# Kernel optimization log

Hardware: AMD Instinct MI355X
Metric: run time of the kernel (lower is better)

The kernel has to match this reference:

```python
import jax, jax.numpy as jnp
import numpy as np

MESH_SIZE = 0.01
TEMP = 0.001
T = 4096
HID = (16, 16, 16)


def _triangle_mesh():
    g = np.arange(-1.0, 1.0 + 1e-9, MESH_SIZE, dtype=np.float32)  # 201 pts
    A, B = np.meshgrid(g, g, indexing='ij')  # alpha rows, beta cols
    mask = A >= B                             # Preisach triangle alpha >= beta
    return A[mask].astype(np.float32), B[mask].astype(np.float32)  # [N], [N]


def _constrain(v, lo, hi):
    return lo + (hi - lo) * jax.nn.sigmoid(v)


def setup_inputs() -> dict:
    key = jax.random.key(0)
    ks = jax.random.split(key, 12)
    alpha_np, beta_np = _triangle_mesh()
    N = alpha_np.shape[0]  # 20301

    def xavier(k, fan_in, fan_out):
        b = np.sqrt(6.0 / (fan_in + fan_out)).astype(np.float32)
        return jax.random.uniform(k, (fan_in, fan_out), jnp.float32, -b, b)

    dims = (2,) + HID + (1,)
    params = {}
    for i in range(4):
        params[f'w{i+1}'] = xavier(ks[i], dims[i], dims[i + 1])
        params[f'b{i+1}'] = jnp.zeros((dims[i + 1],), jnp.float32)

    bound = np.sqrt(6.0 / (1 + N)).astype(np.float32)  # xavier_uniform on (1,N)
    init_state_raw = jax.random.uniform(ks[10], (N,), jnp.float32, -bound, bound)

    return dict(
        x=jax.random.normal(ks[11], (T,), jnp.float32),
        alpha_raw=jnp.asarray(alpha_np),
        beta_raw=jnp.asarray(beta_np),
        init_state_raw=init_state_raw,
        m_scale_raw=jnp.asarray(1.0, jnp.float32),
        m_offset_raw=jnp.asarray(1.0, jnp.float32),
        h_scale_raw=jnp.asarray(1.0, jnp.float32),
        **params,
    )


def _get_states(x, alpha, beta, s0, temp):
    # Soft Preisach relay: switch up where u>alpha, down where u<beta, else hold.
    def step(s, u):
        up = jax.nn.sigmoid((u - alpha) / temp)
        dn = jax.nn.sigmoid((beta - u) / temp)
        s_new = up - dn + (1.0 - up) * (1.0 - dn) * s
        return s_new, s_new
    _, states = jax.lax.scan(step, s0, x)
    return states  # [T, N]


def reference(x, alpha_raw, beta_raw, init_state_raw,
              w1, b1, w2, b2, w3, b3, w4, b4,
              m_scale_raw, m_offset_raw, h_scale_raw):
    alpha = alpha_raw  # ConstrainedParameter with no bounds -> identity
    beta = beta_raw
    s0 = jnp.tanh(init_state_raw)  # BinaryParameter (soft binary)

    states = _get_states(x, alpha, beta, s0, TEMP)  # [T, N]

    mesh = jnp.stack([alpha, beta], axis=1)  # [N, 2]
    h = jax.nn.relu(mesh @ w1 + b1)
    h = jax.nn.relu(h @ w2 + b2)
    h = jax.nn.relu(h @ w3 + b3)
    density = jax.nn.sigmoid(h @ w4 + b4)  # [N, 1]
    density = density.T  # [1, N]

    m = jnp.sum(density * states, axis=-1) / jnp.sum(density, axis=-1)  # [T]

    m_scale = _constrain(m_scale_raw, 0.0, 10.0)
    m_offset = _constrain(m_offset_raw, -10.0, 10.0)
    h_scale = _constrain(h_scale_raw, 0.0, 10.0)

    out = m_scale * m + m_offset + h_scale * x  # [T]
    return out, density, states
```

## Files before the change

### kernel.cpp

```cpp
#include <hip/hip_runtime.h>
#include <math.h>

#define NM 20301
#define TT 4096
#define NC 64
#define CH 64
#define NBLK 80
#define SBLK 20
#define NPROW (SBLK * 4)
#define TPH 16
#define NPH (CH / TPH)
#define LOG2E_K 1442.69504f
#define WNEAR 26.0f

__device__ __forceinline__ void relay_step(float ka, float kb, float ku,
                                           float& aa, float& bb) {
    float z1 = fminf(ka - ku, 63.f);
    float z2 = fminf(ku - kb, 63.f);
    float e1 = __builtin_amdgcn_exp2f(z1);
    float e2 = __builtin_amdgcn_exp2f(z2);
    float p1 = 1.f + e1, p2 = 1.f + e2;
    float r  = __builtin_amdgcn_rcpf(p1 * p2);
    aa = (e2 - e1) * r;
    bb = (e1 * e2) * r;
}

__device__ __forceinline__ float wave_reduce_sum(float w) {
    #pragma unroll
    for (int off = 32; off > 0; off >>= 1)
        w += __shfl_down(w, off, 64);
    return w;
}

__global__ __launch_bounds__(256) void density_kernel(
    const float* __restrict__ alpha, const float* __restrict__ beta,
    const float* __restrict__ w1, const float* __restrict__ b1,
    const float* __restrict__ w2, const float* __restrict__ b2,
    const float* __restrict__ w3, const float* __restrict__ b3,
    const float* __restrict__ w4, const float* __restrict__ b4,
    float* __restrict__ density_out, float* __restrict__ densum_parts,
    float* __restrict__ corr)
{
    int n = blockIdx.x * 256 + threadIdx.x;
    if (n < TT) corr[n] = 0.f;
    bool valid = n < NM;
    int nn = valid ? n : NM - 1;
    float a = alpha[nn], b = beta[nn];

    float h1[16], h2[16], h3[16];
    #pragma unroll
    for (int j = 0; j < 16; j++) {
        float v = fmaf(a, w1[j], fmaf(b, w1[16 + j], b1[j]));
        h1[j] = fmaxf(v, 0.f);
    }
    #pragma unroll
    for (int j = 0; j < 16; j++) {
        float v = b2[j];
        #pragma unroll
        for (int k = 0; k < 16; k++) v = fmaf(h1[k], w2[k * 16 + j], v);
        h2[j] = fmaxf(v, 0.f);
    }
    #pragma unroll
    for (int j = 0; j < 16; j++) {
        float v = b3[j];
        #pragma unroll
        for (int k = 0; k < 16; k++) v = fmaf(h2[k], w3[k * 16 + j], v);
        h3[j] = fmaxf(v, 0.f);
    }
    float v = b4[0];
    #pragma unroll
    for (int k = 0; k < 16; k++) v = fmaf(h3[k], w4[k], v);
    float d = 1.f / (1.f + __expf(-v));

    if (valid) density_out[n] = d;
    float wsum = wave_reduce_sum(valid ? d : 0.f);
    __shared__ float ws_[4];
    if ((threadIdx.x & 63) == 0) ws_[threadIdx.x >> 6] = wsum;
    __syncthreads();
    if (threadIdx.x == 0)
        densum_parts[blockIdx.x] = ws_[0] + ws_[1] + ws_[2] + ws_[3];
}

__global__ __launch_bounds__(256) void states_spec_kernel(
    const float* __restrict__ x, const float* __restrict__ alpha,
    const float* __restrict__ beta, const float* __restrict__ density,
    float* __restrict__ states, float* __restrict__ partials,
    float* __restrict__ Acomp, float* __restrict__ Bcomp)
{
    __shared__ float xs[CH];
    __shared__ float tile[4 * 64 * (TPH + 1)];

    int tid = threadIdx.x;
    int c = blockIdx.y;
    if (tid < CH) xs[tid] = x[c * CH + tid] * LOG2E_K;

    int n0 = blockIdx.x * 1024 + tid;
    float A[4], B[4], d[4], ka[4], kb[4];
    bool v[4];
    #pragma unroll
    for (int q = 0; q < 4; q++) {
        int n = n0 + q * 256;
        v[q] = n < NM;
        int nn = v[q] ? n : NM - 1;
        ka[q] = alpha[nn] * LOG2E_K;
        kb[q] = beta[nn] * LOG2E_K;
        d[q]  = v[q] ? density[n] : 0.f;
        A[q] = 0.f; B[q] = 1.f;
    }
    __syncthreads();

    int wv = tid >> 6, ln = tid & 63;
    int tl = ln & 15, h = ln >> 4;
    float* wtile = &tile[wv * 64 * (TPH + 1)];
    float* tslot = &wtile[ln * (TPH + 1)];
    float* rp    = states + (size_t)c * CH * NM + n0;
    size_t prow  = (size_t)(blockIdx.x * 4 + wv) * TT + c * CH;

    for (int p = 0; p < NPH; p++) {
        float xr[TPH];
        #pragma unroll
        for (int j = 0; j < TPH; j++) xr[j] = xs[p * TPH + j];
        #pragma unroll
        for (int j = 0; j < TPH; j++) {
            float u = xr[j];
            float w1_[4], w2_[4], nr[4];
            #pragma unroll
            for (int q = 0; q < 4; q++) {
                w1_[q] = ka[q] - u;
                w2_[q] = u - kb[q];
                nr[q]  = fminf(fabsf(w1_[q]), fabsf(w2_[q]));
            }
            float nmin = fminf(fminf(nr[0], nr[1]), fminf(nr[2], nr[3]));
            if (__any(nmin < WNEAR)) {
                #pragma unroll
                for (int q = 0; q < 4; q++) {
                    float aa, bb;
                    relay_step(ka[q], kb[q], u, aa, bb);
                    A[q] = fmaf(bb, A[q], aa);
                    B[q] *= bb;
                }
            } else {
                #pragma unroll
                for (int q = 0; q < 4; q++) {
                    bool su = w1_[q] < 0.f, sd = w2_[q] < 0.f;
                    A[q] = su ? 1.f : (sd ? -1.f : A[q]);
                    B[q] = (su || sd) ? 0.f : B[q];
                }
            }
            #pragma unroll
            for (int q = 0; q < 4; q++)
                if (v[q]) rp[q * 256] = A[q];
            rp += NM;
            tslot[j] = fmaf(d[0], A[0], fmaf(d[1], A[1],
                       fmaf(d[2], A[2], d[3] * A[3])));
        }
        asm volatile("s_waitcnt lgkmcnt(0)" ::: "memory");
        float acc = 0.f;
        #pragma unroll
        for (int k = 0; k < TPH; k++)
            acc += wtile[(h * 16 + k) * (TPH + 1) + tl];
        acc += __shfl_xor(acc, 16, 64);
        acc += __shfl_xor(acc, 32, 64);
        if (ln < TPH) partials[prow + p * TPH + ln] = acc;
        asm volatile("s_waitcnt lgkmcnt(0)" ::: "memory");
    }

    #pragma unroll
    for (int q = 0; q < 4; q++) {
        if (v[q]) {
            Acomp[(size_t)c * NM + n0 + q * 256] = A[q];
            Bcomp[(size_t)c * NM + n0 + q * 256] = B[q];
        }
    }
}

__global__ __launch_bounds__(256) void fixup_kernel(
    const float* __restrict__ x, const float* __restrict__ alpha,
    const float* __restrict__ beta, const float* __restrict__ density,
    const float* __restrict__ init_raw,
    const float* __restrict__ Acomp, const float* __restrict__ Bcomp,
    float* __restrict__ states, float* __restrict__ corr)
{
    __shared__ float xs[TT];
    int tid = threadIdx.x;
    for (int i = tid; i < TT; i += 256) xs[i] = x[i] * LOG2E_K;

    int n = blockIdx.x * 256 + tid;
    bool valid = n < NM;
    int nn = valid ? n : NM - 1;
    float ka = alpha[nn] * LOG2E_K;
    float kb = beta[nn] * LOG2E_K;
    float d  = valid ? density[n] : 0.f;
    float s  = tanhf(init_raw[nn]);
    __syncthreads();

    int ln = tid & 63;
    float An = Acomp[nn], Bn = Bcomp[nn];
    for (int c = 0; c < NC; c++) {
        float Ac = An, Bc = Bn;
        if (c + 1 < NC) {
            An = Acomp[(size_t)(c + 1) * NM + nn];
            Bn = Bcomp[(size_t)(c + 1) * NM + nn];
        }
        float Bf = 1.f;
        float ss = s;
        float* rp = states + (size_t)c * CH * NM + n;
        #pragma unroll 1
        for (int j = 0; j < CH; j++) {
            if (!__any(Bf != 0.f)) break;
            float u = xs[c * CH + j];
            float aa, bb;
            relay_step(ka, kb, u, aa, bb);
            Bf *= bb;
            ss = fmaf(bb, ss, aa);
            if (valid && Bf != 0.f) rp[0] = ss;
            float contrib = wave_reduce_sum(d * Bf * s);
            if (ln == 0 && contrib != 0.f) atomicAdd(&corr[c * CH + j], contrib);
            rp += NM;
        }
        s = fmaf(Bc, s, Ac);
    }
}

__global__ __launch_bounds__(256) void finalize_kernel(
    const float* __restrict__ x, const float* __restrict__ partials,
    const float* __restrict__ corr, const float* __restrict__ densum_parts,
    const float* __restrict__ msr, const float* __restrict__ mor,
    const float* __restrict__ hsr, float* __restrict__ out)
{
    int t = blockIdx.x * 256 + threadIdx.x;
    if (t >= TT) return;
    float acc = corr[t];
    for (int r = 0; r < NPROW; r++)
        acc += partials[(size_t)r * TT + t];
    float dsum = 0.f;
    for (int bx = 0; bx < NBLK; bx++)
        dsum += densum_parts[bx];
    float sig_ms = 1.f / (1.f + __expf(-msr[0]));
    float sig_mo = 1.f / (1.f + __expf(-mor[0]));
    float sig_hs = 1.f / (1.f + __expf(-hsr[0]));
    float m_scale  = 10.f * sig_ms;
    float m_offset = fmaf(20.f, sig_mo, -10.f);
    float h_scale  = 10.f * sig_hs;
    float m = acc / dsum;
    out[t] = fmaf(m_scale, m, m_offset) + h_scale * x[t];
}

extern "C" void kernel_launch(void* const* d_in, const int* in_sizes, int n_in,
                              void* d_out, int out_size, void* d_ws, size_t ws_size,
                              hipStream_t stream)
{
    const float* x    = (const float*)d_in[0];
    const float* alpha= (const float*)d_in[1];
    const float* beta = (const float*)d_in[2];
    const float* init = (const float*)d_in[3];
    const float* msr  = (const float*)d_in[4];
    const float* mor  = (const float*)d_in[5];
    const float* hsr  = (const float*)d_in[6];
    const float* w1   = (const float*)d_in[7];
    const float* b1   = (const float*)d_in[8];
    const float* w2   = (const float*)d_in[9];
    const float* b2   = (const float*)d_in[10];
    const float* w3   = (const float*)d_in[11];
    const float* b3   = (const float*)d_in[12];
    const float* w4   = (const float*)d_in[13];
    const float* b4   = (const float*)d_in[14];

    float* out     = (float*)d_out;
    float* density = out + TT;
    float* states  = density + NM;

    float* densum_parts = (float*)d_ws;
    float* corr         = densum_parts + 128;
    float* partials     = corr + TT;
    float* Acomp        = partials + (size_t)NPROW * TT;
    float* Bcomp        = Acomp + (size_t)NC * NM;

    density_kernel<<<dim3(NBLK), dim3(256), 0, stream>>>(
        alpha, beta, w1, b1, w2, b2, w3, b3, w4, b4,
        density, densum_parts, corr);

    states_spec_kernel<<<dim3(SBLK, NC), dim3(256), 0, stream>>>(
        x, alpha, beta, density, states, partials, Acomp, Bcomp);

    fixup_kernel<<<dim3(NBLK), dim3(256), 0, stream>>>(
        x, alpha, beta, density, init, Acomp, Bcomp, states, corr);

    finalize_kernel<<<dim3(TT / 256), dim3(256), 0, stream>>>(
        x, partials, corr, densum_parts, msr, mor, hsr, out);
}
```

Measured before the change: 538.3 us.

## Split serial fixup into chunk-entry scan and parallel per-chunk patch kernel

The old fixup kernel walked all 64 chunks serially per element with only 80 blocks, patching states and using atomics for corrections. It is replaced by a small scan kernel that computes each chunk's entry state from the composed affine maps, followed by a patch kernel launched over a (20,64) grid that fixes every chunk in parallel. Corrections now go into extra partials rows instead of atomics, and finalize sums them. This trades an extra workspace array and one more launch for much more parallelism in the fixup phase.

```diff
diff --git a/kernel.cpp b/kernel.cpp
--- a/kernel.cpp
+++ b/kernel.cpp
@@ -8,6 +8,7 @@
 #define NBLK 80
 #define SBLK 20
 #define NPROW (SBLK * 4)
+#define NROWS (NPROW + 80)
 #define TPH 16
 #define NPH (CH / TPH)
 #define LOG2E_K 1442.69504f
@@ -38,11 +39,9 @@
     const float* __restrict__ w2, const float* __restrict__ b2,
     const float* __restrict__ w3, const float* __restrict__ b3,
     const float* __restrict__ w4, const float* __restrict__ b4,
-    float* __restrict__ density_out, float* __restrict__ densum_parts,
-    float* __restrict__ corr)
+    float* __restrict__ density_out, float* __restrict__ densum_parts)
 {
     int n = blockIdx.x * 256 + threadIdx.x;
-    if (n < TT) corr[n] = 0.f;
     bool valid = n < NM;
     int nn = valid ? n : NM - 1;
     float a = alpha[nn], b = beta[nn];
@@ -116,6 +115,7 @@
     float* rp    = states + (size_t)c * CH * NM + n0;
     size_t prow  = (size_t)(blockIdx.x * 4 + wv) * TT + c * CH;
 
+    #pragma unroll 1
     for (int p = 0; p < NPH; p++) {
         float xr[TPH];
         #pragma unroll
@@ -174,64 +174,111 @@
     }
 }
 
-__global__ __launch_bounds__(256) void fixup_kernel(
+__global__ __launch_bounds__(256) void senter_kernel(
+    const float* __restrict__ init_raw,
+    const float* __restrict__ Acomp, const float* __restrict__ Bcomp,
+    float* __restrict__ senter)
+{
+    int n = blockIdx.x * 256 + threadIdx.x;
+    if (n >= NM) return;
+    float s = tanhf(init_raw[n]);
+    float a0[16], b0[16], a1[16], b1[16];
+    #pragma unroll
+    for (int k = 0; k < 16; k++) {
+        a0[k] = Acomp[(size_t)k * NM + n];
+        b0[k] = Bcomp[(size_t)k * NM + n];
+    }
+    #pragma unroll
+    for (int qtr = 0; qtr < 4; qtr++) {
+        if (qtr < 3) {
+            #pragma unroll
+            for (int k = 0; k < 16; k++) {
+                if (qtr & 1) {
+                    a0[k] = Acomp[(size_t)((qtr + 1) * 16 + k) * NM + n];
+                    b0[k] = Bcomp[(size_t)((qtr + 1) * 16 + k) * NM + n];
+                } else {
+                    a1[k] = Acomp[(size_t)((qtr + 1) * 16 + k) * NM + n];
+                    b1[k] = Bcomp[(size_t)((qtr + 1) * 16 + k) * NM + n];
+                }
+            }
+        }
+        #pragma unroll
+        for (int k = 0; k < 16; k++) {
+            senter[(size_t)(qtr * 16 + k) * NM + n] = s;
+            if (qtr & 1) s = fmaf(b1[k], s, a1[k]);
+            else         s = fmaf(b0[k], s, a0[k]);
+        }
+    }
+}
+
+__global__ __launch_bounds__(256) void patch_kernel(
     const float* __restrict__ x, const float* __restrict__ alpha,
     const float* __restrict__ beta, const float* __restrict__ density,
-    const float* __restrict__ init_raw,
-    const float* __restrict__ Acomp, const float* __restrict__ Bcomp,
-    float* __restrict__ states, float* __restrict__ corr)
-{
-    __shared__ float xs[TT];
+    const float* __restrict__ senter,
+    float* __restrict__ states, float* __restrict__ partials)
+{
+    __shared__ float xsl[CH];
     int tid = threadIdx.x;
-    for (int i = tid; i < TT; i += 256) xs[i] = x[i] * LOG2E_K;
-
-    int n = blockIdx.x * 256 + tid;
-    bool valid = n < NM;
-    int nn = valid ? n : NM - 1;
-    float ka = alpha[nn] * LOG2E_K;
-    float kb = beta[nn] * LOG2E_K;
-    float d  = valid ? density[n] : 0.f;
-    float s  = tanhf(init_raw[nn]);
+    int c = blockIdx.y, bx = blockIdx.x;
+    if (tid < CH) xsl[tid] = x[c * CH + tid] * LOG2E_K;
+
+    int n0 = bx * 1024 + tid;
+    float ka[4], kb[4], d[4], se[4], ss[4], Bf[4];
+    bool v[4];
+    #pragma unroll
+    for (int q = 0; q < 4; q++) {
+        int n = n0 + q * 256;
+        v[q] = n < NM;
+        int nn = v[q] ? n : NM - 1;
+        ka[q] = alpha[nn] * LOG2E_K;
+        kb[q] = beta[nn] * LOG2E_K;
+        d[q]  = v[q] ? density[n] : 0.f;
+        se[q] = senter[(size_t)c * NM + nn];
+        ss[q] = se[q];
+        Bf[q] = 1.f;
+    }
     __syncthreads();
 
-    int ln = tid & 63;
-    float An = Acomp[nn], Bn = Bcomp[nn];
-    for (int c = 0; c < NC; c++) {
-        float Ac = An, Bc = Bn;
-        if (c + 1 < NC) {
-            An = Acomp[(size_t)(c + 1) * NM + nn];
-            Bn = Bcomp[(size_t)(c + 1) * NM + nn];
-        }
-        float Bf = 1.f;
-        float ss = s;
-        float* rp = states + (size_t)c * CH * NM + n;
-        #pragma unroll 1
-        for (int j = 0; j < CH; j++) {
-            if (!__any(Bf != 0.f)) break;
-            float u = xs[c * CH + j];
+    int wv = tid >> 6, ln = tid & 63;
+    float myval = 0.f;
+    float* rp = states + (size_t)c * CH * NM + n0;
+    #pragma unroll 1
+    for (int j = 0; j < CH; j++) {
+        bool live = (Bf[0] != 0.f) | (Bf[1] != 0.f) |
+                    (Bf[2] != 0.f) | (Bf[3] != 0.f);
+        if (!__any(live)) break;
+        float u = xsl[j];
+        float contrib = 0.f;
+        #pragma unroll
+        for (int q = 0; q < 4; q++) {
             float aa, bb;
-            relay_step(ka, kb, u, aa, bb);
-            Bf *= bb;
-            ss = fmaf(bb, ss, aa);
-            if (valid && Bf != 0.f) rp[0] = ss;
-            float contrib = wave_reduce_sum(d * Bf * s);
-            if (ln == 0 && contrib != 0.f) atomicAdd(&corr[c * CH + j], contrib);
-            rp += NM;
-        }
-        s = fmaf(Bc, s, Ac);
-    }
+            relay_step(ka[q], kb[q], u, aa, bb);
+            Bf[q] *= bb;
+            ss[q] = fmaf(bb, ss[q], aa);
+            if (Bf[q] != 0.f) {
+                if (v[q]) rp[q * 256] = ss[q];
+                contrib = fmaf(d[q] * Bf[q], se[q], contrib);
+            }
+        }
+        rp += NM;
+        #pragma unroll
+        for (int off = 1; off < 64; off <<= 1)
+            contrib += __shfl_xor(contrib, off, 64);
+        if (ln == j) myval = contrib;
+    }
+    partials[(size_t)(NPROW + bx * 4 + wv) * TT + c * CH + ln] = myval;
 }
 
 __global__ __launch_bounds__(256) void finalize_kernel(
     const float* __restrict__ x, const float* __restrict__ partials,
-    const float* __restrict__ corr, const float* __restrict__ densum_parts,
+    const float* __restrict__ densum_parts,
     const float* __restrict__ msr, const float* __restrict__ mor,
     const float* __restrict__ hsr, float* __restrict__ out)
 {
     int t = blockIdx.x * 256 + threadIdx.x;
     if (t >= TT) return;
-    float acc = corr[t];
-    for (int r = 0; r < NPROW; r++)
+    float acc = 0.f;
+    for (int r = 0; r < NROWS; r++)
         acc += partials[(size_t)r * TT + t];
     float dsum = 0.f;
     for (int bx = 0; bx < NBLK; bx++)
@@ -271,21 +318,24 @@
     float* states  = density + NM;
 
     float* densum_parts = (float*)d_ws;
-    float* corr         = densum_parts + 128;
-    float* partials     = corr + TT;
-    float* Acomp        = partials + (size_t)NPROW * TT;
+    float* partials     = densum_parts + 128;
+    float* Acomp        = partials + (size_t)NROWS * TT;
     float* Bcomp        = Acomp + (size_t)NC * NM;
+    float* senter       = Bcomp + (size_t)NC * NM;
 
     density_kernel<<<dim3(NBLK), dim3(256), 0, stream>>>(
         alpha, beta, w1, b1, w2, b2, w3, b3, w4, b4,
-        density, densum_parts, corr);
+        density, densum_parts);
 
     states_spec_kernel<<<dim3(SBLK, NC), dim3(256), 0, stream>>>(
         x, alpha, beta, density, states, partials, Acomp, Bcomp);
 
-    fixup_kernel<<<dim3(NBLK), dim3(256), 0, stream>>>(
-        x, alpha, beta, density, init, Acomp, Bcomp, states, corr);
+    senter_kernel<<<dim3(NBLK), dim3(256), 0, stream>>>(
+        init, Acomp, Bcomp, senter);
+
+    patch_kernel<<<dim3(SBLK, NC), dim3(256), 0, stream>>>(
+        x, alpha, beta, density, senter, states, partials);
 
     finalize_kernel<<<dim3(TT / 256), dim3(256), 0, stream>>>(
-        x, partials, corr, densum_parts, msr, mor, hsr, out);
-}
+        x, partials, densum_parts, msr, mor, hsr, out);
+}
```

After: 448.1 us. 16.8% less time.
